# Performance work log

Measured on AMD Instinct MI355X. Metric: run time of the kernel, lower is better.

## Reference

```python
import jax, jax.numpy as jnp
import numpy as np

NQ, NL, QD, LD, H = 100000, 32, 384, 1024, 128
E, E_SEE, E_PRED = 1000000, 750000, 250000
N = NQ + NL
EPS = 1e-5


def _bn(x, g, b):
    # BatchNorm1d in training mode: biased batch statistics over node dim
    mu = x.mean(0)
    var = x.var(0)
    return g * (x - mu) * jax.lax.rsqrt(var + EPS) + b


def _general_conv(x, src, dst, ea, Wm, bm, We, be_):
    # PyG GeneralConv (heads=1, no attention, aggr='add', in==out -> identity skip)
    msg = x[src] @ Wm + bm + ea @ We + be_            # [E_see, H]
    agg = jax.ops.segment_sum(msg, dst, num_segments=N)
    return agg + x


def setup_inputs() -> dict:
    key = jax.random.key(0)
    ks = jax.random.split(key, 20)
    s = lambda fan_in: 1.0 / np.sqrt(fan_in)
    return {
        'query_features': jax.random.normal(ks[0], (NQ, QD), jnp.float32),
        'llm_features': jax.random.normal(ks[1], (NL, LD), jnp.float32),
        'edge_index': jax.random.randint(ks[2], (2, E), 0, N, jnp.int64 if jax.config.jax_enable_x64 else jnp.int32),
        'edge_mask': jax.random.randint(ks[3], (E_PRED,), 0, E),
        'edge_can_see': jax.random.randint(ks[4], (E_SEE,), 0, E),
        'edge_weight': jax.random.uniform(ks[5], (E, 1), jnp.float32),
        'Wq': jax.random.normal(ks[6], (QD, H), jnp.float32) * s(QD),
        'bq': jnp.zeros((H,), jnp.float32),
        'Wl': jax.random.normal(ks[7], (LD, H), jnp.float32) * s(LD),
        'bl': jnp.zeros((H,), jnp.float32),
        'W_em': jax.random.normal(ks[8], (1, 1), jnp.float32),
        'b_em': jnp.zeros((1,), jnp.float32),
        'W1m': jax.random.normal(ks[9], (H, H), jnp.float32) * s(H),
        'b1m': jnp.zeros((H,), jnp.float32),
        'W1e': jax.random.normal(ks[10], (1, H), jnp.float32),
        'b1e': jnp.zeros((H,), jnp.float32),
        'W2m': jax.random.normal(ks[11], (H, H), jnp.float32) * s(H),
        'b2m': jnp.zeros((H,), jnp.float32),
        'W2e': jax.random.normal(ks[12], (1, H), jnp.float32),
        'b2e': jnp.zeros((H,), jnp.float32),
        'g1': jnp.ones((H,), jnp.float32), 'beta1': jnp.zeros((H,), jnp.float32),
        'g2': jnp.ones((H,), jnp.float32), 'beta2': jnp.zeros((H,), jnp.float32),
    }


def reference(query_features, llm_features, edge_index, edge_mask, edge_can_see,
              edge_weight, Wq, bq, Wl, bl, W_em, b_em, W1m, b1m, W1e, b1e,
              W2m, b2m, W2e, b2e, g1, beta1, g2, beta2):
    lrelu = jax.nn.leaky_relu  # slope 0.01 (torch default)
    ei_mask = edge_index[:, edge_can_see]       # [2, E_see]
    ei_pred = edge_index[:, edge_mask]          # [2, E_pred]
    ew = lrelu(edge_weight[edge_can_see] @ W_em + b_em)  # [E_see, 1]
    # feature alignment
    x_ini = jnp.concatenate([query_features @ Wq + bq, llm_features @ Wl + bl], 0)  # [N, H]
    src, dst = ei_mask[0], ei_mask[1]
    x = lrelu(_bn(_general_conv(x_ini, src, dst, ew, W1m, b1m, W1e, b1e), g1, beta1))
    x = _bn(_general_conv(x, src, dst, ew, W2m, b2m, W2e, b2e), g2, beta2)
    edge_predict = jax.nn.sigmoid((x_ini[ei_pred[0]] * x[ei_pred[1]]).mean(-1))  # [E_pred]
    return edge_predict
```

## Files before the change

### kernel.cpp

```cpp
#include <hip/hip_runtime.h>
#include <math.h>

#define NQ 100000
#define NL 32
#define QD 384
#define LD 1024
#define H 128
#define E_TOT 1000000
#define E_SEE 750000
#define E_PRED 250000
#define NN (NQ + NL)
#define EPS 1e-5f

#define NB_SCAN ((NN + 255) / 256)
#define NB_GEMM ((NN + 127) / 128)
#define NB_XINI ((NQ + 127) / 128)

typedef __attribute__((ext_vector_type(8))) short short8;
typedef __attribute__((ext_vector_type(4))) short short4v;
typedef __attribute__((ext_vector_type(4))) float f32x4;

__device__ __forceinline__ unsigned short f2bf(float f) {
  unsigned int u = __builtin_bit_cast(unsigned int, f);
  u = (u + 0x7FFFu + ((u >> 16) & 1u)) >> 16;
  return (unsigned short)u;
}


__global__ void k_ew_hist(const int* __restrict__ ecs, const int* __restrict__ EI,
                          const float* __restrict__ ewt, const float* __restrict__ Wem,
                          const float* __restrict__ bem, float* __restrict__ ew,
                          int* __restrict__ cnt) {
  int e = blockIdx.x * 256 + threadIdx.x;
  if (e >= E_SEE) return;
  int idx = ecs[e];
  int d = EI[E_TOT + idx];
  atomicAdd(&cnt[d], 1);
  float w = ewt[idx] * Wem[0] + bem[0];
  ew[e] = w > 0.f ? w : 0.01f * w;
}

__global__ void k_scan_block(const int* __restrict__ cnt, int* __restrict__ bsum) {
  __shared__ int red[256];
  int i = blockIdx.x * 256 + threadIdx.x;
  red[threadIdx.x] = (i < NN) ? cnt[i] : 0;
  __syncthreads();
  for (int s = 128; s > 0; s >>= 1) {
    if (threadIdx.x < s) red[threadIdx.x] += red[threadIdx.x + s];
    __syncthreads();
  }
  if (threadIdx.x == 0) bsum[blockIdx.x] = red[0];
}

__global__ void k_scan_top(const int* __restrict__ bsum, int* __restrict__ boff) {
  __shared__ int buf[2][512];
  int t = threadIdx.x;
  int v = (t < NB_SCAN) ? bsum[t] : 0;
  buf[0][t] = v;
  __syncthreads();
  int src = 0;
  for (int d = 1; d < 512; d <<= 1) {
    int x = buf[src][t];
    if (t >= d) x += buf[src][t - d];
    buf[src ^ 1][t] = x;
    __syncthreads();
    src ^= 1;
  }
  if (t < NB_SCAN) boff[t] = buf[src][t] - v;
}

__global__ void k_scan_write(const int* __restrict__ cnt, const int* __restrict__ boff,
                             int* __restrict__ off) {
  __shared__ int buf[2][256];
  int t = threadIdx.x;
  int i = blockIdx.x * 256 + t;
  int v = (i < NN) ? cnt[i] : 0;
  buf[0][t] = v;
  __syncthreads();
  int src = 0;
  for (int d = 1; d < 256; d <<= 1) {
    int x = buf[src][t];
    if (t >= d) x += buf[src][t - d];
    buf[src ^ 1][t] = x;
    __syncthreads();
    src ^= 1;
  }
  if (i < NN) off[i] = boff[blockIdx.x] + buf[src][t] - v;
  if (i == 0) off[NN] = E_SEE;
}

__global__ void k_fill(const int* __restrict__ ecs, const int* __restrict__ EI,
                       const float* __restrict__ ew, const int* __restrict__ off,
                       int* __restrict__ cur, int* __restrict__ csr_src,
                       float* __restrict__ csr_ew) {
  int e = blockIdx.x * 256 + threadIdx.x;
  if (e >= E_SEE) return;
  int idx = ecs[e];
  int s = EI[idx];
  int d = EI[E_TOT + idx];
  int p = off[d] + atomicAdd(&cur[d], 1);
  csr_src[p] = s;
  csr_ew[p] = ew[e];
}


__global__ void k_prep_wqt(const float* __restrict__ Wq, unsigned short* __restrict__ Wqt) {
  for (int i = blockIdx.x * 256 + threadIdx.x; i < QD * H; i += gridDim.x * 256) {
    int n = i / QD, k = i - n * QD;
    Wqt[i] = f2bf(Wq[(size_t)k * H + n]);
  }
}


__global__ __launch_bounds__(256) void k_xini(
    const float* __restrict__ qf, const float* __restrict__ lf,
    const unsigned short* __restrict__ Wqt, const float* __restrict__ bq,
    const float* __restrict__ Wl, const float* __restrict__ bl,
    float* __restrict__ XINI) {
  if ((int)blockIdx.x < NB_XINI) {
    __shared__ unsigned short sA[128][40];
    __shared__ unsigned short sB[128][40];
    int tid = threadIdx.x;
    int w = tid >> 6, lane = tid & 63;
    int l15 = lane & 15, quad = lane >> 4;
    int wr = (w >> 1) * 64, wc = (w & 1) * 64;
    int rowbase = blockIdx.x * 128;
    f32x4 acc[4][4];
#pragma unroll
    for (int i = 0; i < 4; i++)
#pragma unroll
      for (int j = 0; j < 4; j++) acc[i][j] = (f32x4){0.f, 0.f, 0.f, 0.f};

    for (int kb = 0; kb < QD; kb += 32) {
#pragma unroll
      for (int pass = 0; pass < 4; ++pass) {
        int row = pass * 32 + (tid >> 3);
        int kc = (tid & 7) * 4;
        int gr = rowbase + row;
        float4 v = make_float4(0.f, 0.f, 0.f, 0.f);
        if (gr < NQ) v = *(const float4*)&qf[(size_t)gr * QD + kb + kc];
        short4v b;
        b.x = (short)f2bf(v.x); b.y = (short)f2bf(v.y);
        b.z = (short)f2bf(v.z); b.w = (short)f2bf(v.w);
        *(short4v*)&sA[row][kc] = b;
      }
#pragma unroll
      for (int pass = 0; pass < 2; ++pass) {
        int n = pass * 64 + (tid >> 2);
        int k8 = (tid & 3) * 8;
        *(int4*)&sB[n][k8] = *(const int4*)&Wqt[(size_t)n * QD + kb + k8];
      }
      __syncthreads();
      short8 af[4], bfr[4];
#pragma unroll
      for (int mt = 0; mt < 4; ++mt)
        af[mt] = *(const short8*)&sA[wr + mt * 16 + l15][quad * 8];
#pragma unroll
      for (int nt = 0; nt < 4; ++nt)
        bfr[nt] = *(const short8*)&sB[wc + nt * 16 + l15][quad * 8];
#pragma unroll
      for (int mt = 0; mt < 4; ++mt)
#pragma unroll
        for (int nt = 0; nt < 4; ++nt)
          acc[mt][nt] = __builtin_amdgcn_mfma_f32_16x16x32_bf16(
              af[mt], bfr[nt], acc[mt][nt], 0, 0, 0);
      __syncthreads();
    }
#pragma unroll
    for (int nt = 0; nt < 4; ++nt) {
      int col = wc + nt * 16 + l15;
      float bias = bq[col];
#pragma unroll
      for (int mt = 0; mt < 4; ++mt) {
#pragma unroll
        for (int r = 0; r < 4; ++r) {
          int n = rowbase + wr + mt * 16 + quad * 4 + r;
          if (n < NQ) XINI[(size_t)n * H + col] = acc[mt][nt][r] + bias;
        }
      }
    }
  } else {
    int r = blockIdx.x - NB_XINI;
    int t = threadIdx.x;
    if (r >= NL || t >= H) return;
    float acc = 0.f;
    for (int k = 0; k < LD; k += 4) {
      float a0 = lf[(size_t)r * LD + k + 0];
      float a1 = lf[(size_t)r * LD + k + 1];
      float a2 = lf[(size_t)r * LD + k + 2];
      float a3 = lf[(size_t)r * LD + k + 3];
      acc = fmaf(a0, Wl[(size_t)(k + 0) * H + t], acc);
      acc = fmaf(a1, Wl[(size_t)(k + 1) * H + t], acc);
      acc = fmaf(a2, Wl[(size_t)(k + 2) * H + t], acc);
      acc = fmaf(a3, Wl[(size_t)(k + 3) * H + t], acc);
    }
    XINI[(size_t)(NQ + r) * H + t] = acc + bl[t];
  }
}


template <bool TRANS>
__global__ __launch_bounds__(256) void k_seg(
    const float* __restrict__ Xin, const int* __restrict__ off,
    const int* __restrict__ csr_src, const float* __restrict__ csr_ew,
    const float* __restrict__ scale, const float* __restrict__ shift,
    float* __restrict__ S, float* __restrict__ swsum, float* __restrict__ degf) {
  int w = blockIdx.x * 4 + (threadIdx.x >> 6);
  if (w >= NN) return;
  int lane = threadIdx.x & 63;
  int o0 = off[w], o1 = off[w + 1];
  float ax = 1.f, ay = 1.f, bx = 0.f, by = 0.f;
  if (TRANS) {
    float2 sc = *(const float2*)&scale[lane * 2];
    float2 sh = *(const float2*)&shift[lane * 2];
    ax = sc.x; ay = sc.y; bx = sh.x; by = sh.y;
  }
  float accx = 0.f, accy = 0.f, ews = 0.f;
  for (int k = o0; k < o1; ++k) {
    int s = csr_src[k];
    float2 v = *(const float2*)&Xin[(size_t)s * H + lane * 2];
    if (TRANS) {
      float t0 = fmaf(ax, v.x, bx); v.x = t0 > 0.f ? t0 : 0.01f * t0;
      float t1 = fmaf(ay, v.y, by); v.y = t1 > 0.f ? t1 : 0.01f * t1;
    }
    accx += v.x; accy += v.y;
    ews += csr_ew[k];
  }
  *(float2*)&S[(size_t)w * H + lane * 2] = make_float2(accx, accy);
  if (lane == 0) { swsum[w] = ews; degf[w] = (float)(o1 - o0); }
}


template <bool TRANS>
__global__ __launch_bounds__(256) void k_gemm(
    const float* __restrict__ S, const float* __restrict__ Xin,
    float* __restrict__ Xout, const float* __restrict__ W,
    const float* __restrict__ bm, const float* __restrict__ be,
    const float* __restrict__ We,
    const float* __restrict__ scale, const float* __restrict__ shift,
    const float* __restrict__ swsum, const float* __restrict__ degf,
    float* __restrict__ partials) {
  __shared__ float sA[16][132];
  __shared__ float sB[16][128];
  __shared__ float st[2][16][128];
  int tid = threadIdx.x;
  int tx = tid & 15, ty = tid >> 4;
  int rowbase = blockIdx.x * 128;
  float c[8][8];
#pragma unroll
  for (int i = 0; i < 8; i++)
#pragma unroll
    for (int j = 0; j < 8; j++) c[i][j] = 0.f;
  for (int kb = 0; kb < H; kb += 16) {
#pragma unroll
    for (int p = 0; p < 2; ++p) {
      int f = tid + p * 256;
      int row = f >> 2;
      int kq = (f & 3) << 2;
      int gr = rowbase + row;
      float4 v = make_float4(0.f, 0.f, 0.f, 0.f);
      if (gr < NN) v = *(const float4*)&S[(size_t)gr * H + kb + kq];
      sA[kq + 0][row] = v.x; sA[kq + 1][row] = v.y;
      sA[kq + 2][row] = v.z; sA[kq + 3][row] = v.w;
    }
#pragma unroll
    for (int p = 0; p < 2; ++p) {
      int f = tid + p * 256;
      int k = f >> 5;
      int cq = (f & 31) << 2;
      *(float4*)&sB[k][cq] = *(const float4*)&W[(size_t)(kb + k) * H + cq];
    }
    __syncthreads();
#pragma unroll
    for (int k = 0; k < 16; ++k) {
      float4 a0 = *(const float4*)&sA[k][ty * 8];
      float4 a1 = *(const float4*)&sA[k][ty * 8 + 4];
      float4 b0 = *(const float4*)&sB[k][tx * 8];
      float4 b1 = *(const float4*)&sB[k][tx * 8 + 4];
      float av[8] = {a0.x, a0.y, a0.z, a0.w, a1.x, a1.y, a1.z, a1.w};
      float bv[8] = {b0.x, b0.y, b0.z, b0.w, b1.x, b1.y, b1.z, b1.w};
#pragma unroll
      for (int i = 0; i < 8; i++)
#pragma unroll
        for (int j = 0; j < 8; j++) c[i][j] = fmaf(av[i], bv[j], c[i][j]);
    }
    __syncthreads();
  }
  int c0 = tx * 8;
  float cb[8], we[8], sc[8], sh[8];
  {
    float4 m0 = *(const float4*)&bm[c0];
    float4 m1 = *(const float4*)&bm[c0 + 4];
    float4 e0 = *(const float4*)&be[c0];
    float4 e1 = *(const float4*)&be[c0 + 4];
    cb[0] = m0.x + e0.x; cb[1] = m0.y + e0.y; cb[2] = m0.z + e0.z; cb[3] = m0.w + e0.w;
    cb[4] = m1.x + e1.x; cb[5] = m1.y + e1.y; cb[6] = m1.z + e1.z; cb[7] = m1.w + e1.w;
    float4 w0 = *(const float4*)&We[c0];
    float4 w1 = *(const float4*)&We[c0 + 4];
    we[0] = w0.x; we[1] = w0.y; we[2] = w0.z; we[3] = w0.w;
    we[4] = w1.x; we[5] = w1.y; we[6] = w1.z; we[7] = w1.w;
    if (TRANS) {
      float4 s0 = *(const float4*)&scale[c0];
      float4 s1 = *(const float4*)&scale[c0 + 4];
      float4 h0 = *(const float4*)&shift[c0];
      float4 h1 = *(const float4*)&shift[c0 + 4];
      sc[0] = s0.x; sc[1] = s0.y; sc[2] = s0.z; sc[3] = s0.w;
      sc[4] = s1.x; sc[5] = s1.y; sc[6] = s1.z; sc[7] = s1.w;
      sh[0] = h0.x; sh[1] = h0.y; sh[2] = h0.z; sh[3] = h0.w;
      sh[4] = h1.x; sh[5] = h1.y; sh[6] = h1.z; sh[7] = h1.w;
    }
  }
  float ps[8], pss[8];
#pragma unroll
  for (int j = 0; j < 8; j++) { ps[j] = 0.f; pss[j] = 0.f; }
#pragma unroll
  for (int i = 0; i < 8; i++) {
    int n = rowbase + ty * 8 + i;
    if (n < NN) {
      float dg = degf[n], sw = swsum[n];
      float4 r0 = *(const float4*)&Xin[(size_t)n * H + c0];
      float4 r1 = *(const float4*)&Xin[(size_t)n * H + c0 + 4];
      float rr[8] = {r0.x, r0.y, r0.z, r0.w, r1.x, r1.y, r1.z, r1.w};
      if (TRANS) {
#pragma unroll
        for (int j = 0; j < 8; j++) {
          float t = fmaf(sc[j], rr[j], sh[j]);
          rr[j] = t > 0.f ? t : 0.01f * t;
        }
      }
      float o[8];
#pragma unroll
      for (int j = 0; j < 8; j++) {
        o[j] = c[i][j] + dg * cb[j] + sw * we[j] + rr[j];
        ps[j] += o[j];
        pss[j] += o[j] * o[j];
      }
      *(float4*)&Xout[(size_t)n * H + c0] = make_float4(o[0], o[1], o[2], o[3]);
      *(float4*)&Xout[(size_t)n * H + c0 + 4] = make_float4(o[4], o[5], o[6], o[7]);
    }
  }
  *(float4*)&st[0][ty][c0] = make_float4(ps[0], ps[1], ps[2], ps[3]);
  *(float4*)&st[0][ty][c0 + 4] = make_float4(ps[4], ps[5], ps[6], ps[7]);
  *(float4*)&st[1][ty][c0] = make_float4(pss[0], pss[1], pss[2], pss[3]);
  *(float4*)&st[1][ty][c0 + 4] = make_float4(pss[4], pss[5], pss[6], pss[7]);
  __syncthreads();
  int stt = tid >> 7, col = tid & 127;
  float s = 0.f;
#pragma unroll
  for (int y = 0; y < 16; y++) s += st[stt][y][col];
  partials[(size_t)blockIdx.x * 256 + tid] = s;
}


__global__ void k_bnstats(const float* __restrict__ partials,
                          const float* __restrict__ g, const float* __restrict__ beta,
                          float* __restrict__ scale, float* __restrict__ shift) {
  __shared__ float s[256];
  int t = threadIdx.x;
  float acc = 0.f;
  for (int b = 0; b < NB_GEMM; ++b) acc += partials[(size_t)b * 256 + t];
  s[t] = acc;
  __syncthreads();
  if (t < H) {
    float mean = s[t] / (float)NN;
    float var = s[128 + t] / (float)NN - mean * mean;
    float a = g[t] * rsqrtf(var + EPS);
    scale[t] = a;
    shift[t] = beta[t] - mean * a;
  }
}


__global__ __launch_bounds__(256) void k_pred(
    const int* __restrict__ emask, const int* __restrict__ EI,
    const float* __restrict__ XINI, const float* __restrict__ X,
    const float* __restrict__ scale, const float* __restrict__ shift,
    float* __restrict__ out) {
  int i = blockIdx.x * 4 + (threadIdx.x >> 6);
  if (i >= E_PRED) return;
  int lane = threadIdx.x & 63;
  int m = emask[i];
  int p0 = EI[m];
  int p1 = EI[E_TOT + m];
  float2 a = *(const float2*)&XINI[(size_t)p0 * H + lane * 2];
  float2 b = *(const float2*)&X[(size_t)p1 * H + lane * 2];
  float2 sc = *(const float2*)&scale[lane * 2];
  float2 sh = *(const float2*)&shift[lane * 2];
  float v = a.x * fmaf(sc.x, b.x, sh.x) + a.y * fmaf(sc.y, b.y, sh.y);
#pragma unroll
  for (int mm = 32; mm > 0; mm >>= 1) v += __shfl_xor(v, mm, 64);
  if (lane == 0) out[i] = 1.f / (1.f + expf(-v * (1.f / 128.f)));
}


extern "C" void kernel_launch(void* const* d_in, const int* in_sizes, int n_in,
                              void* d_out, int out_size, void* d_ws, size_t ws_size,
                              hipStream_t stream) {
  const float* qf    = (const float*)d_in[0];
  const float* lf    = (const float*)d_in[1];
  const int*   EI    = (const int*)d_in[2];
  const int*   emask = (const int*)d_in[3];
  const int*   ecs   = (const int*)d_in[4];
  const float* ewt   = (const float*)d_in[5];
  const float* Wq    = (const float*)d_in[6];
  const float* bq    = (const float*)d_in[7];
  const float* Wl    = (const float*)d_in[8];
  const float* bl    = (const float*)d_in[9];
  const float* Wem   = (const float*)d_in[10];
  const float* bem   = (const float*)d_in[11];
  const float* W1m   = (const float*)d_in[12];
  const float* b1m   = (const float*)d_in[13];
  const float* W1e   = (const float*)d_in[14];
  const float* b1e   = (const float*)d_in[15];
  const float* W2m   = (const float*)d_in[16];
  const float* b2m   = (const float*)d_in[17];
  const float* W2e   = (const float*)d_in[18];
  const float* b2e   = (const float*)d_in[19];
  const float* g1    = (const float*)d_in[20];
  const float* beta1 = (const float*)d_in[21];
  const float* g2    = (const float*)d_in[22];
  const float* beta2 = (const float*)d_in[23];
  float* out = (float*)d_out;

  char* p = (char*)d_ws;
  auto alloc = [&](size_t bytes) -> void* {
    void* r = (void*)p;
    p += (bytes + 255) & ~(size_t)255;
    return r;
  };
  float* XINI    = (float*)alloc((size_t)NN * H * 4);
  float* X       = (float*)alloc((size_t)NN * H * 4);
  float* S       = (float*)alloc((size_t)NN * H * 4);
  float* ew      = (float*)alloc((size_t)E_SEE * 4);
  float* csr_ew  = (float*)alloc((size_t)E_SEE * 4);
  int*   csr_src = (int*)alloc((size_t)E_SEE * 4);
  int*   cnt     = (int*)alloc((size_t)NN * 4);
  int*   off     = (int*)alloc((size_t)(NN + 1) * 4);
  int*   cur     = (int*)alloc((size_t)NN * 4);
  int*   bsum    = (int*)alloc((size_t)NB_SCAN * 4);
  int*   boff    = (int*)alloc((size_t)NB_SCAN * 4);
  float* swsum   = (float*)alloc((size_t)NN * 4);
  float* degf    = (float*)alloc((size_t)NN * 4);
  float* partials= (float*)alloc((size_t)NB_GEMM * 256 * 4);
  float* scale1  = (float*)alloc(128 * 4);
  float* shift1  = (float*)alloc(128 * 4);
  float* scale2  = (float*)alloc(128 * 4);
  float* shift2  = (float*)alloc(128 * 4);
  unsigned short* Wqt = (unsigned short*)alloc((size_t)QD * H * 2);

  hipMemsetAsync(cnt, 0, (size_t)NN * 4, stream);
  hipMemsetAsync(cur, 0, (size_t)NN * 4, stream);

  int ebl = (E_SEE + 255) / 256;
  k_prep_wqt<<<48, 256, 0, stream>>>(Wq, Wqt);
  k_ew_hist<<<ebl, 256, 0, stream>>>(ecs, EI, ewt, Wem, bem, ew, cnt);
  k_scan_block<<<NB_SCAN, 256, 0, stream>>>(cnt, bsum);
  k_scan_top<<<1, 512, 0, stream>>>(bsum, boff);
  k_scan_write<<<NB_SCAN, 256, 0, stream>>>(cnt, boff, off);
  k_fill<<<ebl, 256, 0, stream>>>(ecs, EI, ew, off, cur, csr_src, csr_ew);

  k_xini<<<NB_XINI + NL, 256, 0, stream>>>(qf, lf, Wqt, bq, Wl, bl, XINI);

  int segbl = (NN + 3) / 4;
  k_seg<false><<<segbl, 256, 0, stream>>>(XINI, off, csr_src, csr_ew,
                                          nullptr, nullptr, S, swsum, degf);
  k_gemm<false><<<NB_GEMM, 256, 0, stream>>>(S, XINI, X, W1m, b1m, b1e, W1e,
                                             nullptr, nullptr, swsum, degf, partials);
  k_bnstats<<<1, 256, 0, stream>>>(partials, g1, beta1, scale1, shift1);
  k_seg<true><<<segbl, 256, 0, stream>>>(X, off, csr_src, csr_ew,
                                         scale1, shift1, S, swsum, degf);
  k_gemm<true><<<NB_GEMM, 256, 0, stream>>>(S, X, X, W2m, b2m, b2e, W2e,
                                            scale1, shift1, swsum, degf, partials);
  k_bnstats<<<1, 256, 0, stream>>>(partials, g2, beta2, scale2, shift2);
  int pbl = (E_PRED + 3) / 4;
  k_pred<<<pbl, 256, 0, stream>>>(emask, EI, XINI, X, scale2, shift2, out);
}
```

Baseline: 825.1 us.

## Move GCN GEMMs to bf16 MFMA, parallelize BN stats and LLM projection

The fp32 FMA GEMMs in both GeneralConv layers become bf16 MFMA tiles, with the segment-sum output S stored as bf16 and the weights pre-transposed to bf16 in one prep kernel. The query projection GEMM now register-prefetches the next K slice while computing the current one. The LLM projection moves from 32 single blocks inside k_xini to a split-K kernel plus a combine kernel. BN statistics reduce across 128 blocks instead of one. The bf16 storage of S cuts memory traffic but adds rounding error to the aggregated messages.

Result: faster. 724.5 us (-12.2%).

```diff
diff --git a/kernel.cpp b/kernel.cpp
--- a/kernel.cpp
+++ b/kernel.cpp
@@ -104,97 +104,143 @@
 }
 
 
-__global__ void k_prep_wqt(const float* __restrict__ Wq, unsigned short* __restrict__ Wqt) {
-  for (int i = blockIdx.x * 256 + threadIdx.x; i < QD * H; i += gridDim.x * 256) {
+__global__ void k_prep(const float* __restrict__ Wq, const float* __restrict__ W1m,
+                       const float* __restrict__ W2m,
+                       unsigned short* __restrict__ Wqt, unsigned short* __restrict__ W1t,
+                       unsigned short* __restrict__ W2t) {
+  int i = blockIdx.x * 256 + threadIdx.x;
+  const int tot1 = QD * H;
+  const int tot2 = H * H;
+  if (i < tot1) {
     int n = i / QD, k = i - n * QD;
     Wqt[i] = f2bf(Wq[(size_t)k * H + n]);
-  }
+  } else if (i < tot1 + tot2) {
+    int j = i - tot1;
+    int n = j >> 7, k = j & 127;
+    W1t[j] = f2bf(W1m[(size_t)k * H + n]);
+  } else if (i < tot1 + 2 * tot2) {
+    int j = i - tot1 - tot2;
+    int n = j >> 7, k = j & 127;
+    W2t[j] = f2bf(W2m[(size_t)k * H + n]);
+  }
+}
+
+
+__global__ __launch_bounds__(128) void k_llm_part(const float* __restrict__ lf,
+                                                  const float* __restrict__ Wl,
+                                                  float* __restrict__ part) {
+  int r = blockIdx.x >> 3;
+  int s = blockIdx.x & 7;
+  int t = threadIdx.x;
+  int k0 = s * 128;
+  float acc = 0.f;
+#pragma unroll 4
+  for (int k = 0; k < 128; k += 4) {
+    float a0 = lf[(size_t)r * LD + k0 + k + 0];
+    float a1 = lf[(size_t)r * LD + k0 + k + 1];
+    float a2 = lf[(size_t)r * LD + k0 + k + 2];
+    float a3 = lf[(size_t)r * LD + k0 + k + 3];
+    acc = fmaf(a0, Wl[(size_t)(k0 + k + 0) * H + t], acc);
+    acc = fmaf(a1, Wl[(size_t)(k0 + k + 1) * H + t], acc);
+    acc = fmaf(a2, Wl[(size_t)(k0 + k + 2) * H + t], acc);
+    acc = fmaf(a3, Wl[(size_t)(k0 + k + 3) * H + t], acc);
+  }
+  part[(size_t)blockIdx.x * 128 + t] = acc;
+}
+
+__global__ void k_llm_comb(const float* __restrict__ part, const float* __restrict__ bl,
+                           float* __restrict__ XINI) {
+  int i = blockIdx.x * 256 + threadIdx.x;
+  if (i >= NL * H) return;
+  int r = i >> 7, t = i & 127;
+  float a = bl[t];
+#pragma unroll
+  for (int s = 0; s < 8; s++) a += part[(size_t)(r * 8 + s) * 128 + t];
+  XINI[(size_t)(NQ + r) * H + t] = a;
 }
 
 
 __global__ __launch_bounds__(256) void k_xini(
-    const float* __restrict__ qf, const float* __restrict__ lf,
-    const unsigned short* __restrict__ Wqt, const float* __restrict__ bq,
-    const float* __restrict__ Wl, const float* __restrict__ bl,
-    float* __restrict__ XINI) {
-  if ((int)blockIdx.x < NB_XINI) {
-    __shared__ unsigned short sA[128][40];
-    __shared__ unsigned short sB[128][40];
-    int tid = threadIdx.x;
-    int w = tid >> 6, lane = tid & 63;
-    int l15 = lane & 15, quad = lane >> 4;
-    int wr = (w >> 1) * 64, wc = (w & 1) * 64;
-    int rowbase = blockIdx.x * 128;
-    f32x4 acc[4][4];
-#pragma unroll
-    for (int i = 0; i < 4; i++)
-#pragma unroll
-      for (int j = 0; j < 4; j++) acc[i][j] = (f32x4){0.f, 0.f, 0.f, 0.f};
-
-    for (int kb = 0; kb < QD; kb += 32) {
-#pragma unroll
-      for (int pass = 0; pass < 4; ++pass) {
-        int row = pass * 32 + (tid >> 3);
-        int kc = (tid & 7) * 4;
-        int gr = rowbase + row;
-        float4 v = make_float4(0.f, 0.f, 0.f, 0.f);
-        if (gr < NQ) v = *(const float4*)&qf[(size_t)gr * QD + kb + kc];
-        short4v b;
-        b.x = (short)f2bf(v.x); b.y = (short)f2bf(v.y);
-        b.z = (short)f2bf(v.z); b.w = (short)f2bf(v.w);
-        *(short4v*)&sA[row][kc] = b;
+    const float* __restrict__ qf, const unsigned short* __restrict__ Wqt,
+    const float* __restrict__ bq, float* __restrict__ XINI) {
+  __shared__ unsigned short sA[128][40];
+  __shared__ unsigned short sB[128][40];
+  int tid = threadIdx.x;
+  int w = tid >> 6, lane = tid & 63;
+  int l15 = lane & 15, quad = lane >> 4;
+  int wr = (w >> 1) * 64, wc = (w & 1) * 64;
+  int rowbase = blockIdx.x * 128;
+  f32x4 acc[4][4];
+#pragma unroll
+  for (int i = 0; i < 4; i++)
+#pragma unroll
+    for (int j = 0; j < 4; j++) acc[i][j] = (f32x4){0.f, 0.f, 0.f, 0.f};
+
+  int arow = tid >> 3, akc = (tid & 7) * 4;
+  int bn = tid >> 2, bk8 = (tid & 3) * 8;
+  float4 pa[4];
+  int4 pb[2];
+#pragma unroll
+  for (int p = 0; p < 4; ++p) {
+    int gr = rowbase + p * 32 + arow;
+    pa[p] = (gr < NQ) ? *(const float4*)&qf[(size_t)gr * QD + akc]
+                      : make_float4(0.f, 0.f, 0.f, 0.f);
+  }
+#pragma unroll
+  for (int p = 0; p < 2; ++p)
+    pb[p] = *(const int4*)&Wqt[(size_t)(p * 64 + bn) * QD + bk8];
+
+  for (int step = 0; step < 12; ++step) {
+    int kb = step * 32;
+#pragma unroll
+    for (int p = 0; p < 4; ++p) {
+      short4v b;
+      b.x = (short)f2bf(pa[p].x); b.y = (short)f2bf(pa[p].y);
+      b.z = (short)f2bf(pa[p].z); b.w = (short)f2bf(pa[p].w);
+      *(short4v*)&sA[p * 32 + arow][akc] = b;
+    }
+#pragma unroll
+    for (int p = 0; p < 2; ++p) *(int4*)&sB[p * 64 + bn][bk8] = pb[p];
+    __syncthreads();
+    if (step + 1 < 12) {
+      int kn = kb + 32;
+#pragma unroll
+      for (int p = 0; p < 4; ++p) {
+        int gr = rowbase + p * 32 + arow;
+        pa[p] = (gr < NQ) ? *(const float4*)&qf[(size_t)gr * QD + kn + akc]
+                          : make_float4(0.f, 0.f, 0.f, 0.f);
       }
 #pragma unroll
-      for (int pass = 0; pass < 2; ++pass) {
-        int n = pass * 64 + (tid >> 2);
-        int k8 = (tid & 3) * 8;
-        *(int4*)&sB[n][k8] = *(const int4*)&Wqt[(size_t)n * QD + kb + k8];
+      for (int p = 0; p < 2; ++p)
+        pb[p] = *(const int4*)&Wqt[(size_t)(p * 64 + bn) * QD + kn + bk8];
+    }
+    short8 af[4], bfr[4];
+#pragma unroll
+    for (int mt = 0; mt < 4; ++mt)
+      af[mt] = *(const short8*)&sA[wr + mt * 16 + l15][quad * 8];
+#pragma unroll
+    for (int nt = 0; nt < 4; ++nt)
+      bfr[nt] = *(const short8*)&sB[wc + nt * 16 + l15][quad * 8];
+#pragma unroll
+    for (int mt = 0; mt < 4; ++mt)
+#pragma unroll
+      for (int nt = 0; nt < 4; ++nt)
+        acc[mt][nt] = __builtin_amdgcn_mfma_f32_16x16x32_bf16(
+            af[mt], bfr[nt], acc[mt][nt], 0, 0, 0);
+    __syncthreads();
+  }
+#pragma unroll
+  for (int nt = 0; nt < 4; ++nt) {
+    int col = wc + nt * 16 + l15;
+    float bias = bq[col];
+#pragma unroll
+    for (int mt = 0; mt < 4; ++mt) {
+#pragma unroll
+      for (int r = 0; r < 4; ++r) {
+        int n = rowbase + wr + mt * 16 + quad * 4 + r;
+        if (n < NQ) XINI[(size_t)n * H + col] = acc[mt][nt][r] + bias;
       }
-      __syncthreads();
-      short8 af[4], bfr[4];
-#pragma unroll
-      for (int mt = 0; mt < 4; ++mt)
-        af[mt] = *(const short8*)&sA[wr + mt * 16 + l15][quad * 8];
-#pragma unroll
-      for (int nt = 0; nt < 4; ++nt)
-        bfr[nt] = *(const short8*)&sB[wc + nt * 16 + l15][quad * 8];
-#pragma unroll
-      for (int mt = 0; mt < 4; ++mt)
-#pragma unroll
-        for (int nt = 0; nt < 4; ++nt)
-          acc[mt][nt] = __builtin_amdgcn_mfma_f32_16x16x32_bf16(
-              af[mt], bfr[nt], acc[mt][nt], 0, 0, 0);
-      __syncthreads();
-    }
-#pragma unroll
-    for (int nt = 0; nt < 4; ++nt) {
-      int col = wc + nt * 16 + l15;
-      float bias = bq[col];
-#pragma unroll
-      for (int mt = 0; mt < 4; ++mt) {
-#pragma unroll
-        for (int r = 0; r < 4; ++r) {
-          int n = rowbase + wr + mt * 16 + quad * 4 + r;
-          if (n < NQ) XINI[(size_t)n * H + col] = acc[mt][nt][r] + bias;
-        }
-      }
-    }
-  } else {
-    int r = blockIdx.x - NB_XINI;
-    int t = threadIdx.x;
-    if (r >= NL || t >= H) return;
-    float acc = 0.f;
-    for (int k = 0; k < LD; k += 4) {
-      float a0 = lf[(size_t)r * LD + k + 0];
-      float a1 = lf[(size_t)r * LD + k + 1];
-      float a2 = lf[(size_t)r * LD + k + 2];
-      float a3 = lf[(size_t)r * LD + k + 3];
-      acc = fmaf(a0, Wl[(size_t)(k + 0) * H + t], acc);
-      acc = fmaf(a1, Wl[(size_t)(k + 1) * H + t], acc);
-      acc = fmaf(a2, Wl[(size_t)(k + 2) * H + t], acc);
-      acc = fmaf(a3, Wl[(size_t)(k + 3) * H + t], acc);
-    }
-    XINI[(size_t)(NQ + r) * H + t] = acc + bl[t];
+    }
   }
 }
 
@@ -204,7 +250,8 @@
     const float* __restrict__ Xin, const int* __restrict__ off,
     const int* __restrict__ csr_src, const float* __restrict__ csr_ew,
     const float* __restrict__ scale, const float* __restrict__ shift,
-    float* __restrict__ S, float* __restrict__ swsum, float* __restrict__ degf) {
+    unsigned short* __restrict__ S16, float* __restrict__ swsum,
+    float* __restrict__ degf) {
   int w = blockIdx.x * 4 + (threadIdx.x >> 6);
   if (w >= NN) return;
   int lane = threadIdx.x & 63;
@@ -226,147 +273,152 @@
     accx += v.x; accy += v.y;
     ews += csr_ew[k];
   }
-  *(float2*)&S[(size_t)w * H + lane * 2] = make_float2(accx, accy);
+  unsigned int pk = ((unsigned int)f2bf(accy) << 16) | f2bf(accx);
+  *(unsigned int*)&S16[(size_t)w * H + lane * 2] = pk;
   if (lane == 0) { swsum[w] = ews; degf[w] = (float)(o1 - o0); }
 }
 
 
 template <bool TRANS>
 __global__ __launch_bounds__(256) void k_gemm(
-    const float* __restrict__ S, const float* __restrict__ Xin,
-    float* __restrict__ Xout, const float* __restrict__ W,
+    const unsigned short* __restrict__ S16, const float* __restrict__ Xin,
+    float* __restrict__ Xout, const unsigned short* __restrict__ Wt,
     const float* __restrict__ bm, const float* __restrict__ be,
     const float* __restrict__ We,
     const float* __restrict__ scale, const float* __restrict__ shift,
     const float* __restrict__ swsum, const float* __restrict__ degf,
     float* __restrict__ partials) {
-  __shared__ float sA[16][132];
-  __shared__ float sB[16][128];
-  __shared__ float st[2][16][128];
+  __shared__ unsigned short sA[128][40];
+  __shared__ unsigned short sB[128][40];
+  __shared__ float st[2][8][128];
   int tid = threadIdx.x;
-  int tx = tid & 15, ty = tid >> 4;
+  int w = tid >> 6, lane = tid & 63;
+  int l15 = lane & 15, quad = lane >> 4;
+  int wr = (w >> 1) * 64, wc = (w & 1) * 64;
   int rowbase = blockIdx.x * 128;
-  float c[8][8];
-#pragma unroll
-  for (int i = 0; i < 8; i++)
-#pragma unroll
-    for (int j = 0; j < 8; j++) c[i][j] = 0.f;
-  for (int kb = 0; kb < H; kb += 16) {
-#pragma unroll
-    for (int p = 0; p < 2; ++p) {
-      int f = tid + p * 256;
-      int row = f >> 2;
-      int kq = (f & 3) << 2;
-      int gr = rowbase + row;
-      float4 v = make_float4(0.f, 0.f, 0.f, 0.f);
-      if (gr < NN) v = *(const float4*)&S[(size_t)gr * H + kb + kq];
-      sA[kq + 0][row] = v.x; sA[kq + 1][row] = v.y;
-      sA[kq + 2][row] = v.z; sA[kq + 3][row] = v.w;
-    }
-#pragma unroll
-    for (int p = 0; p < 2; ++p) {
-      int f = tid + p * 256;
-      int k = f >> 5;
-      int cq = (f & 31) << 2;
-      *(float4*)&sB[k][cq] = *(const float4*)&W[(size_t)(kb + k) * H + cq];
-    }
-    __syncthreads();
-#pragma unroll
-    for (int k = 0; k < 16; ++k) {
-      float4 a0 = *(const float4*)&sA[k][ty * 8];
-      float4 a1 = *(const float4*)&sA[k][ty * 8 + 4];
-      float4 b0 = *(const float4*)&sB[k][tx * 8];
-      float4 b1 = *(const float4*)&sB[k][tx * 8 + 4];
-      float av[8] = {a0.x, a0.y, a0.z, a0.w, a1.x, a1.y, a1.z, a1.w};
-      float bv[8] = {b0.x, b0.y, b0.z, b0.w, b1.x, b1.y, b1.z, b1.w};
-#pragma unroll
-      for (int i = 0; i < 8; i++)
-#pragma unroll
-        for (int j = 0; j < 8; j++) c[i][j] = fmaf(av[i], bv[j], c[i][j]);
-    }
-    __syncthreads();
-  }
-  int c0 = tx * 8;
-  float cb[8], we[8], sc[8], sh[8];
+  f32x4 acc[4][4];
+#pragma unroll
+  for (int i = 0; i < 4; i++)
+#pragma unroll
+    for (int j = 0; j < 4; j++) acc[i][j] = (f32x4){0.f, 0.f, 0.f, 0.f};
+
+  int arow = tid >> 1, ah = (tid & 1) * 16;
+  int4 pa[2], pb[2];
   {
-    float4 m0 = *(const float4*)&bm[c0];
-    float4 m1 = *(const float4*)&bm[c0 + 4];
-    float4 e0 = *(const float4*)&be[c0];
-    float4 e1 = *(const float4*)&be[c0 + 4];
-    cb[0] = m0.x + e0.x; cb[1] = m0.y + e0.y; cb[2] = m0.z + e0.z; cb[3] = m0.w + e0.w;
-    cb[4] = m1.x + e1.x; cb[5] = m1.y + e1.y; cb[6] = m1.z + e1.z; cb[7] = m1.w + e1.w;
-    float4 w0 = *(const float4*)&We[c0];
-    float4 w1 = *(const float4*)&We[c0 + 4];
-    we[0] = w0.x; we[1] = w0.y; we[2] = w0.z; we[3] = w0.w;
-    we[4] = w1.x; we[5] = w1.y; we[6] = w1.z; we[7] = w1.w;
-    if (TRANS) {
-      float4 s0 = *(const float4*)&scale[c0];
-      float4 s1 = *(const float4*)&scale[c0 + 4];
-      float4 h0 = *(const float4*)&shift[c0];
-      float4 h1 = *(const float4*)&shift[c0 + 4];
-      sc[0] = s0.x; sc[1] = s0.y; sc[2] = s0.z; sc[3] = s0.w;
-      sc[4] = s1.x; sc[5] = s1.y; sc[6] = s1.z; sc[7] = s1.w;
-      sh[0] = h0.x; sh[1] = h0.y; sh[2] = h0.z; sh[3] = h0.w;
-      sh[4] = h1.x; sh[5] = h1.y; sh[6] = h1.z; sh[7] = h1.w;
-    }
-  }
-  float ps[8], pss[8];
-#pragma unroll
-  for (int j = 0; j < 8; j++) { ps[j] = 0.f; pss[j] = 0.f; }
-#pragma unroll
-  for (int i = 0; i < 8; i++) {
-    int n = rowbase + ty * 8 + i;
-    if (n < NN) {
-      float dg = degf[n], sw = swsum[n];
-      float4 r0 = *(const float4*)&Xin[(size_t)n * H + c0];
-      float4 r1 = *(const float4*)&Xin[(size_t)n * H + c0 + 4];
-      float rr[8] = {r0.x, r0.y, r0.z, r0.w, r1.x, r1.y, r1.z, r1.w};
-      if (TRANS) {
-#pragma unroll
-        for (int j = 0; j < 8; j++) {
-          float t = fmaf(sc[j], rr[j], sh[j]);
-          rr[j] = t > 0.f ? t : 0.01f * t;
+    int gr = rowbase + arow;
+    if (gr < NN) {
+      pa[0] = *(const int4*)&S16[(size_t)gr * H + ah];
+      pa[1] = *(const int4*)&S16[(size_t)gr * H + ah + 8];
+    } else {
+      pa[0] = make_int4(0, 0, 0, 0); pa[1] = make_int4(0, 0, 0, 0);
+    }
+    pb[0] = *(const int4*)&Wt[(size_t)arow * H + ah];
+    pb[1] = *(const int4*)&Wt[(size_t)arow * H + ah + 8];
+  }
+  for (int step = 0; step < 4; ++step) {
+    *(int4*)&sA[arow][ah] = pa[0];
+    *(int4*)&sA[arow][ah + 8] = pa[1];
+    *(int4*)&sB[arow][ah] = pb[0];
+    *(int4*)&sB[arow][ah + 8] = pb[1];
+    __syncthreads();
+    if (step + 1 < 4) {
+      int kn = (step + 1) * 32;
+      int gr = rowbase + arow;
+      if (gr < NN) {
+        pa[0] = *(const int4*)&S16[(size_t)gr * H + kn + ah];
+        pa[1] = *(const int4*)&S16[(size_t)gr * H + kn + ah + 8];
+      } else {
+        pa[0] = make_int4(0, 0, 0, 0); pa[1] = make_int4(0, 0, 0, 0);
+      }
+      pb[0] = *(const int4*)&Wt[(size_t)arow * H + kn + ah];
+      pb[1] = *(const int4*)&Wt[(size_t)arow * H + kn + ah + 8];
+    }
+    short8 af[4], bfr[4];
+#pragma unroll
+    for (int mt = 0; mt < 4; ++mt)
+      af[mt] = *(const short8*)&sA[wr + mt * 16 + l15][quad * 8];
+#pragma unroll
+    for (int nt = 0; nt < 4; ++nt)
+      bfr[nt] = *(const short8*)&sB[wc + nt * 16 + l15][quad * 8];
+#pragma unroll
+    for (int mt = 0; mt < 4; ++mt)
+#pragma unroll
+      for (int nt = 0; nt < 4; ++nt)
+        acc[mt][nt] = __builtin_amdgcn_mfma_f32_16x16x32_bf16(
+            af[mt], bfr[nt], acc[mt][nt], 0, 0, 0);
+    __syncthreads();
+  }
+  int col4[4];
+  float cb4[4], we4[4], sc4[4], sh4[4], ps[4], pq[4];
+#pragma unroll
+  for (int nt = 0; nt < 4; ++nt) {
+    int col = wc + nt * 16 + l15;
+    col4[nt] = col;
+    cb4[nt] = bm[col] + be[col];
+    we4[nt] = We[col];
+    if (TRANS) { sc4[nt] = scale[col]; sh4[nt] = shift[col]; }
+    ps[nt] = 0.f; pq[nt] = 0.f;
+  }
+#pragma unroll
+  for (int mt = 0; mt < 4; ++mt) {
+#pragma unroll
+    for (int r = 0; r < 4; ++r) {
+      int n = rowbase + wr + mt * 16 + quad * 4 + r;
+      if (n < NN) {
+        float dg = degf[n], sw = swsum[n];
+#pragma unroll
+        for (int nt = 0; nt < 4; ++nt) {
+          float rr = Xin[(size_t)n * H + col4[nt]];
+          if (TRANS) {
+            float t = fmaf(sc4[nt], rr, sh4[nt]);
+            rr = t > 0.f ? t : 0.01f * t;
+          }
+          float o = acc[mt][nt][r] + dg * cb4[nt] + sw * we4[nt] + rr;
+          Xout[(size_t)n * H + col4[nt]] = o;
+          ps[nt] += o; pq[nt] += o * o;
         }
       }
-      float o[8];
-#pragma unroll
-      for (int j = 0; j < 8; j++) {
-        o[j] = c[i][j] + dg * cb[j] + sw * we[j] + rr[j];
-        ps[j] += o[j];
-        pss[j] += o[j] * o[j];
-      }
-      *(float4*)&Xout[(size_t)n * H + c0] = make_float4(o[0], o[1], o[2], o[3]);
-      *(float4*)&Xout[(size_t)n * H + c0 + 4] = make_float4(o[4], o[5], o[6], o[7]);
-    }
-  }
-  *(float4*)&st[0][ty][c0] = make_float4(ps[0], ps[1], ps[2], ps[3]);
-  *(float4*)&st[0][ty][c0 + 4] = make_float4(ps[4], ps[5], ps[6], ps[7]);
-  *(float4*)&st[1][ty][c0] = make_float4(pss[0], pss[1], pss[2], pss[3]);
-  *(float4*)&st[1][ty][c0 + 4] = make_float4(pss[4], pss[5], pss[6], pss[7]);
+    }
+  }
+  int slot = (w >> 1) * 4 + quad;
+#pragma unroll
+  for (int nt = 0; nt < 4; ++nt) {
+    st[0][slot][col4[nt]] = ps[nt];
+    st[1][slot][col4[nt]] = pq[nt];
+  }
   __syncthreads();
-  int stt = tid >> 7, col = tid & 127;
+  int plane = tid >> 7, col = tid & 127;
   float s = 0.f;
 #pragma unroll
-  for (int y = 0; y < 16; y++) s += st[stt][y][col];
+  for (int y = 0; y < 8; y++) s += st[plane][y][col];
   partials[(size_t)blockIdx.x * 256 + tid] = s;
 }
 
 
-__global__ void k_bnstats(const float* __restrict__ partials,
-                          const float* __restrict__ g, const float* __restrict__ beta,
-                          float* __restrict__ scale, float* __restrict__ shift) {
-  __shared__ float s[256];
+__global__ __launch_bounds__(256) void k_bnstats(
+    const float* __restrict__ partials, const float* __restrict__ g,
+    const float* __restrict__ beta, float* __restrict__ scale,
+    float* __restrict__ shift) {
+  __shared__ float rs[256], rq[256];
+  int j = blockIdx.x;
   int t = threadIdx.x;
-  float acc = 0.f;
-  for (int b = 0; b < NB_GEMM; ++b) acc += partials[(size_t)b * 256 + t];
-  s[t] = acc;
+  float as = 0.f, aq = 0.f;
+  for (int b = t; b < NB_GEMM; b += 256) {
+    as += partials[(size_t)b * 256 + j];
+    aq += partials[(size_t)b * 256 + 128 + j];
+  }
+  rs[t] = as; rq[t] = aq;
   __syncthreads();
-  if (t < H) {
-    float mean = s[t] / (float)NN;
-    float var = s[128 + t] / (float)NN - mean * mean;
-    float a = g[t] * rsqrtf(var + EPS);
-    scale[t] = a;
-    shift[t] = beta[t] - mean * a;
+  for (int s = 128; s > 0; s >>= 1) {
+    if (t < s) { rs[t] += rs[t + s]; rq[t] += rq[t + s]; }
+    __syncthreads();
+  }
+  if (t == 0) {
+    float mean = rs[0] / (float)NN;
+    float var = rq[0] / (float)NN - mean * mean;
+    float a = g[j] * rsqrtf(var + EPS);
+    scale[j] = a;
+    shift[j] = beta[j] - mean * a;
   }
 }
 
@@ -430,7 +482,7 @@
   };
   float* XINI    = (float*)alloc((size_t)NN * H * 4);
   float* X       = (float*)alloc((size_t)NN * H * 4);
-  float* S       = (float*)alloc((size_t)NN * H * 4);
+  unsigned short* S16 = (unsigned short*)alloc((size_t)NN * H * 2);
   float* ew      = (float*)alloc((size_t)E_SEE * 4);
   float* csr_ew  = (float*)alloc((size_t)E_SEE * 4);
   int*   csr_src = (int*)alloc((size_t)E_SEE * 4);
@@ -447,31 +499,36 @@
   float* scale2  = (float*)alloc(128 * 4);
   float* shift2  = (float*)alloc(128 * 4);
   unsigned short* Wqt = (unsigned short*)alloc((size_t)QD * H * 2);
+  unsigned short* W1t = (unsigned short*)alloc((size_t)H * H * 2);
+  unsigned short* W2t = (unsigned short*)alloc((size_t)H * H * 2);
+  float* llmpart = (float*)alloc((size_t)NL * 8 * H * 4);
 
   hipMemsetAsync(cnt, 0, (size_t)NN * 4, stream);
   hipMemsetAsync(cur, 0, (size_t)NN * 4, stream);
 
   int ebl = (E_SEE + 255) / 256;
-  k_prep_wqt<<<48, 256, 0, stream>>>(Wq, Wqt);
+  k_prep<<<320, 256, 0, stream>>>(Wq, W1m, W2m, Wqt, W1t, W2t);
   k_ew_hist<<<ebl, 256, 0, stream>>>(ecs, EI, ewt, Wem, bem, ew, cnt);
   k_scan_block<<<NB_SCAN, 256, 0, stream>>>(cnt, bsum);
   k_scan_top<<<1, 512, 0, stream>>>(bsum, boff);
   k_scan_write<<<NB_SCAN, 256, 0, stream>>>(cnt, boff, off);
   k_fill<<<ebl, 256, 0, stream>>>(ecs, EI, ew, off, cur, csr_src, csr_ew);
 
-  k_xini<<<NB_XINI + NL, 256, 0, stream>>>(qf, lf, Wqt, bq, Wl, bl, XINI);
+  k_llm_part<<<NL * 8, 128, 0, stream>>>(lf, Wl, llmpart);
+  k_llm_comb<<<(NL * H + 255) / 256, 256, 0, stream>>>(llmpart, bl, XINI);
+  k_xini<<<NB_XINI, 256, 0, stream>>>(qf, Wqt, bq, XINI);
 
   int segbl = (NN + 3) / 4;
   k_seg<false><<<segbl, 256, 0, stream>>>(XINI, off, csr_src, csr_ew,
-                                          nullptr, nullptr, S, swsum, degf);
-  k_gemm<false><<<NB_GEMM, 256, 0, stream>>>(S, XINI, X, W1m, b1m, b1e, W1e,
+                                          nullptr, nullptr, S16, swsum, degf);
+  k_gemm<false><<<NB_GEMM, 256, 0, stream>>>(S16, XINI, X, W1t, b1m, b1e, W1e,
                                              nullptr, nullptr, swsum, degf, partials);
-  k_bnstats<<<1, 256, 0, stream>>>(partials, g1, beta1, scale1, shift1);
+  k_bnstats<<<H, 256, 0, stream>>>(partials, g1, beta1, scale1, shift1);
   k_seg<true><<<segbl, 256, 0, stream>>>(X, off, csr_src, csr_ew,
-                                         scale1, shift1, S, swsum, degf);
-  k_gemm<true><<<NB_GEMM, 256, 0, stream>>>(S, X, X, W2m, b2m, b2e, W2e,
+                                         scale1, shift1, S16, swsum, degf);
+  k_gemm<true><<<NB_GEMM, 256, 0, stream>>>(S16, X, X, W2t, b2m, b2e, W2e,
                                             scale1, shift1, swsum, degf, partials);
-  k_bnstats<<<1, 256, 0, stream>>>(partials, g2, beta2, scale2, shift2);
+  k_bnstats<<<H, 256, 0, stream>>>(partials, g2, beta2, scale2, shift2);
   int pbl = (E_PRED + 3) / 4;
   k_pred<<<pbl, 256, 0, stream>>>(emask, EI, XINI, X, scale2, shift2, out);
 }
```
